# Kernel optimization log

Hardware: AMD Instinct MI355X
Metric: run time of the kernel (lower is better)

The kernel has to match this reference:

```python
import jax, jax.numpy as jnp
import numpy as np

N = 50000      # nodes
E = 800000     # edges (before self loops)
IN, H, OUT = 128, 64, 64
NEG_SLOPE = 0.2  # PyG GATConv leaky_relu slope


def _glorot(k, shape):
    lim = float(np.sqrt(6.0 / (shape[0] + shape[1])))
    return jax.random.uniform(k, shape, jnp.float32, -lim, lim)


def setup_inputs() -> dict:
    key = jax.random.key(0)
    ks = jax.random.split(key, 16)
    x = jax.random.normal(ks[0], (N, IN), jnp.float32)
    edge_src = jax.random.randint(ks[1], (E,), 0, N, jnp.int32)
    edge_dst = jax.random.randint(ks[2], (E,), 0, N, jnp.int32)
    dims = [(IN, H), (H, H), (H, OUT)]
    inp = {"x": x, "edge_src": edge_src, "edge_dst": edge_dst}
    i = 3
    for l, (di, do) in enumerate(dims):
        inp[f"W{l}"] = _glorot(ks[i], (di, do)); i += 1
        inp[f"as{l}"] = _glorot(ks[i], (1, do))[0]; i += 1
        inp[f"ad{l}"] = _glorot(ks[i], (1, do))[0]; i += 1
        inp[f"b{l}"] = jnp.zeros((do,), jnp.float32)
    return inp


def _gat_layer(x, W, a_src, a_dst, b, src, dst):
    # single-head GATConv (PyG semantics, self loops already in src/dst)
    h = x @ W                              # [N, do]
    s = h @ a_src                          # [N] source attention logits
    d = h @ a_dst                          # [N] dest attention logits
    e = jax.nn.leaky_relu(s[src] + d[dst], NEG_SLOPE)   # [E']
    # segment softmax over incoming edges of each destination node
    m = jax.ops.segment_max(e, dst, num_segments=N)
    w = jnp.exp(e - m[dst])
    denom = jax.ops.segment_sum(w, dst, num_segments=N)
    coef = w / (denom[dst] + 1e-16)
    out = jax.ops.segment_sum(h[src] * coef[:, None], dst, num_segments=N)
    return out + b


def reference(x, edge_src, edge_dst, W0, as0, ad0, b0, W1, as1, ad1, b1, W2, as2, ad2, b2):
    # add self loops (GATConv default add_self_loops=True)
    loop = jnp.arange(N, dtype=edge_src.dtype)
    src = jnp.concatenate([edge_src, loop])
    dst = jnp.concatenate([edge_dst, loop])
    h = jax.nn.relu(_gat_layer(x, W0, as0, ad0, b0, src, dst))
    # dropout is identity in eval mode
    h = jax.nn.relu(_gat_layer(h, W1, as1, ad1, b1, src, dst))
    return _gat_layer(h, W2, as2, ad2, b2, src, dst)
```

## Files before the change

### kernel.cpp

```cpp
#include <hip/hip_runtime.h>
#include <hip/hip_fp16.h>
#include <math.h>

#define WAVE 64
#define NEG_SLOPE 0.2f
#define LSTR 68


__global__ __launch_bounds__(256) void bucket_count_kernel(
    const int* __restrict__ dst, int* __restrict__ gcnt, int e, int nb) {
    extern __shared__ int cnt[];
    for (int b = threadIdx.x; b < nb; b += 256) cnt[b] = 0;
    __syncthreads();
    int base = blockIdx.x * 4096;
#pragma unroll
    for (int k = 0; k < 16; ++k) {
        int i = base + k * 256 + threadIdx.x;
        if (i < e) atomicAdd(&cnt[dst[i] >> 7], 1);
    }
    __syncthreads();
    for (int b = threadIdx.x; b < nb; b += 256) {
        int c = cnt[b];
        if (c) atomicAdd(&gcnt[b], c);
    }
}

__global__ __launch_bounds__(512) void bucket_scan_kernel(
    const int* __restrict__ gcnt, int* __restrict__ boff, int* __restrict__ gfill,
    int* __restrict__ rowptr, int nb, int e, int n) {
    __shared__ int sh[512];
    int t = threadIdx.x;
    int v = (t < nb) ? gcnt[t] : 0;
    sh[t] = v;
    __syncthreads();
    for (int o = 1; o < 512; o <<= 1) {
        int u = (t >= o) ? sh[t - o] : 0;
        __syncthreads();
        sh[t] += u;
        __syncthreads();
    }
    if (t < nb) { int ex = sh[t] - v; boff[t] = ex; gfill[t] = ex; }
    if (t == 0) { boff[nb] = e; rowptr[n] = e + n; }
}

__global__ __launch_bounds__(256) void bucket_place_kernel(
    const int* __restrict__ src, const int* __restrict__ dst,
    int* __restrict__ gfill, int* __restrict__ binned, int e, int nb) {
    extern __shared__ int lds[];
    int* cnt = lds;
    int* bas = lds + nb;
    for (int b = threadIdx.x; b < nb; b += 256) cnt[b] = 0;
    __syncthreads();
    int base = blockIdx.x * 4096;
#pragma unroll
    for (int k = 0; k < 16; ++k) {
        int i = base + k * 256 + threadIdx.x;
        if (i < e) atomicAdd(&cnt[dst[i] >> 7], 1);
    }
    __syncthreads();
    for (int b = threadIdx.x; b < nb; b += 256) {
        int c = cnt[b];
        bas[b] = c ? atomicAdd(&gfill[b], c) : 0;
        cnt[b] = 0;
    }
    __syncthreads();
#pragma unroll
    for (int k = 0; k < 16; ++k) {
        int i = base + k * 256 + threadIdx.x;
        if (i < e) {
            int d = dst[i];
            int bk = d >> 7;
            int r = atomicAdd(&cnt[bk], 1);
            binned[bas[bk] + r] = ((d & 127) << 16) | src[i];
        }
    }
}

__global__ __launch_bounds__(256) void bucket_build_kernel(
    const int* __restrict__ binned, const int* __restrict__ boff,
    int* __restrict__ csr_src, int* __restrict__ rowptr, int n) {
    __shared__ int cnt[128], off[128], pcnt[128];
    int b = blockIdx.x;
    int t = threadIdx.x;
    int nodeBase = b << 7;
    int nc = min(128, n - nodeBase);
    int e0 = boff[b], e1 = boff[b + 1];
    int ne = e1 - e0;
    if (t < 128) { cnt[t] = 1; pcnt[t] = 1; }
    __syncthreads();
    for (int i = t; i < ne; i += 256)
        atomicAdd(&cnt[binned[e0 + i] >> 16], 1);
    __syncthreads();
    if (t < 128) off[t] = cnt[t];
    __syncthreads();
    for (int o = 1; o < 128; o <<= 1) {
        int u = (t >= o && t < 128) ? off[t - o] : 0;
        __syncthreads();
        if (t < 128) off[t] += u;
        __syncthreads();
    }
    if (t < 128) off[t] -= cnt[t];
    __syncthreads();
    int csrBase = e0 + nodeBase;
    if (t < nc) {
        rowptr[nodeBase + t] = csrBase + off[t];
        csr_src[csrBase + off[t]] = nodeBase + t;
    }
    for (int i = t; i < ne; i += 256) {
        int p = binned[e0 + i];
        int loc = p >> 16;
        int r = atomicAdd(&pcnt[loc], 1);
        csr_src[csrBase + off[loc] + r] = p & 0xFFFF;
    }
}


template <int K>
__global__ __launch_bounds__(256) void gemm_feat_kernel(
    const float* __restrict__ X, const float* __restrict__ W,
    const float* __restrict__ a_s, const float* __restrict__ a_d,
    __half* __restrict__ H, float* __restrict__ S, float* __restrict__ D, int n) {
    __shared__ float Xs[64 * LSTR];
    __shared__ float Ws[64 * LSTR];
    int t = threadIdx.x;
    int tx = t & 15;
    int ty = t >> 4;
    int base = blockIdx.x * 64;
    float acc[4][4] = {};

    int q = t & 3;
    int srow = t >> 2;

    for (int k0 = 0; k0 < K; k0 += 64) {
        int grow = base + srow;
#pragma unroll
        for (int j = 0; j < 4; ++j) {
            int c = 16 * j + 4 * q;
            float4 v = make_float4(0.f, 0.f, 0.f, 0.f);
            if (grow < n) v = *(const float4*)(X + (size_t)grow * K + k0 + c);
            *(float4*)(Xs + srow * LSTR + c) = v;
            float4 w = *(const float4*)(W + (size_t)(k0 + srow) * 64 + c);
            *(float4*)(Ws + srow * LSTR + c) = w;
        }
        __syncthreads();
#pragma unroll 8
        for (int kk = 0; kk < 64; ++kk) {
            float4 wv = *(const float4*)(Ws + kk * LSTR + 4 * tx);
#pragma unroll
            for (int i = 0; i < 4; ++i) {
                float xv = Xs[(4 * ty + i) * LSTR + kk];
                acc[i][0] = fmaf(xv, wv.x, acc[i][0]);
                acc[i][1] = fmaf(xv, wv.y, acc[i][1]);
                acc[i][2] = fmaf(xv, wv.z, acc[i][2]);
                acc[i][3] = fmaf(xv, wv.w, acc[i][3]);
            }
        }
        __syncthreads();
    }

    const float4 av_s = *(const float4*)(a_s + 4 * tx);
    const float4 av_d = *(const float4*)(a_d + 4 * tx);
#pragma unroll
    for (int i = 0; i < 4; ++i) {
        int row = base + 4 * ty + i;
        bool ok = row < n;
        if (ok) {
            __half2 h01 = __floats2half2_rn(acc[i][0], acc[i][1]);
            __half2 h23 = __floats2half2_rn(acc[i][2], acc[i][3]);
            uint2 u;
            u.x = *(unsigned int*)&h01;
            u.y = *(unsigned int*)&h23;
            *(uint2*)(H + (size_t)row * 64 + 4 * tx) = u;
        }
        float ps = acc[i][0] * av_s.x + acc[i][1] * av_s.y +
                   acc[i][2] * av_s.z + acc[i][3] * av_s.w;
        float pd = acc[i][0] * av_d.x + acc[i][1] * av_d.y +
                   acc[i][2] * av_d.z + acc[i][3] * av_d.w;
        for (int o = 1; o < 16; o <<= 1) {
            ps += __shfl_xor(ps, o);
            pd += __shfl_xor(pd, o);
        }
        if (tx == 0 && ok) { S[row] = ps; D[row] = pd; }
    }
}


__global__ __launch_bounds__(256) void gat_aggregate_kernel(
    const __half* __restrict__ H, const float* __restrict__ S,
    const float* __restrict__ D, const int* __restrict__ rowptr,
    const int* __restrict__ csr_src, const float* __restrict__ bias,
    float* __restrict__ OUT, int n, int do_relu) {
    int wid  = (blockIdx.x * blockDim.x + threadIdx.x) >> 6;
    int lane = threadIdx.x & 63;
    if (wid >= n) return;
    int eg = lane >> 4;
    int cg = lane & 15;
    int start = rowptr[wid];
    int end   = rowptr[wid + 1];
    float d_i = D[wid];

    float z = 0.f;
    float4 acc = make_float4(0.f, 0.f, 0.f, 0.f);

    for (int cb = start; cb < end; cb += WAVE) {
        int j = cb + lane;
        bool v = j < end;
        int sc = v ? csr_src[j] : 0;
        float sv = S[sc];
        float e = sv + d_i;
        e = (e > 0.f) ? e : NEG_SLOPE * e;
        float w = v ? __expf(e) : 0.f;

        int nch = min(WAVE, end - cb);
        int rounds = (nch + 3) >> 2;
#pragma unroll 4
        for (int r = 0; r < rounds; ++r) {
            int idx = 4 * r + eg;
            float wr = __shfl(w, idx);
            int   sr = __shfl(sc, idx);
            float2 f0 = make_float2(0.f, 0.f), f1 = f0;
            if (idx < nch) {
                uint2 u = *(const uint2*)(H + (size_t)sr * 64 + 4 * cg);
                f0 = __half22float2(*(__half2*)&u.x);
                f1 = __half22float2(*(__half2*)&u.y);
            }
            z += wr;
            acc.x = fmaf(wr, f0.x, acc.x);
            acc.y = fmaf(wr, f0.y, acc.y);
            acc.z = fmaf(wr, f1.x, acc.z);
            acc.w = fmaf(wr, f1.y, acc.w);
        }
    }

    for (int o = 16; o < 64; o <<= 1) {
        acc.x += __shfl_xor(acc.x, o);
        acc.y += __shfl_xor(acc.y, o);
        acc.z += __shfl_xor(acc.z, o);
        acc.w += __shfl_xor(acc.w, o);
        z     += __shfl_xor(z, o);
    }

    if (eg == 0) {
        float inv = 1.f / (z + 1e-16f);
        const float4 bv = *(const float4*)(bias + 4 * cg);
        float4 o4;
        o4.x = acc.x * inv + bv.x;
        o4.y = acc.y * inv + bv.y;
        o4.z = acc.z * inv + bv.z;
        o4.w = acc.w * inv + bv.w;
        if (do_relu) {
            o4.x = fmaxf(o4.x, 0.f); o4.y = fmaxf(o4.y, 0.f);
            o4.z = fmaxf(o4.z, 0.f); o4.w = fmaxf(o4.w, 0.f);
        }
        *(float4*)(OUT + (size_t)wid * 64 + 4 * cg) = o4;
    }
}


static inline size_t align256(size_t x) { return (x + 255) & ~(size_t)255; }

extern "C" void kernel_launch(void* const* d_in, const int* in_sizes, int n_in,
                              void* d_out, int out_size, void* d_ws, size_t ws_size,
                              hipStream_t stream) {
    const float* x    = (const float*)d_in[0];
    const int*   esrc = (const int*)d_in[1];
    const int*   edst = (const int*)d_in[2];
    const int E = in_sizes[1];
    const int N = in_sizes[0] / 128;

    const float* W0 = (const float*)d_in[3];
    const float* as0 = (const float*)d_in[4];
    const float* ad0 = (const float*)d_in[5];
    const float* b0 = (const float*)d_in[6];
    const float* W1 = (const float*)d_in[7];
    const float* as1 = (const float*)d_in[8];
    const float* ad1 = (const float*)d_in[9];
    const float* b1 = (const float*)d_in[10];
    const float* W2 = (const float*)d_in[11];
    const float* as2 = (const float*)d_in[12];
    const float* ad2 = (const float*)d_in[13];
    const float* b2 = (const float*)d_in[14];

    const int NB = (N + 127) >> 7;

    char* p = (char*)d_ws;
    int* gcnt    = (int*)p; p += align256((size_t)(NB + 1) * 4);
    int* boff    = (int*)p; p += align256((size_t)(NB + 1) * 4);
    int* gfill   = (int*)p; p += align256((size_t)(NB + 1) * 4);
    int* rowptr  = (int*)p; p += align256((size_t)(N + 1) * 4);
    int* csr_src = (int*)p; p += align256((size_t)(E + N) * 4);
    int* binned  = (int*)p; p += align256((size_t)E * 4);
    __half* h16 = (__half*)p; p += align256((size_t)N * 64 * 2);
    float* sA = (float*)p; p += align256((size_t)N * 4);
    float* dA = (float*)p; p += align256((size_t)N * 4);
    float* XA = (float*)p; p += align256((size_t)N * 64 * 4);
    float* XB = (float*)p; p += align256((size_t)N * 64 * 4);
    float* out = (float*)d_out;

    int nchunk = (E + 4095) / 4096;
    hipMemsetAsync(gcnt, 0, (size_t)(NB + 1) * 4, stream);
    bucket_count_kernel<<<nchunk, 256, NB * 4, stream>>>(edst, gcnt, E, NB);
    bucket_scan_kernel<<<1, 512, 0, stream>>>(gcnt, boff, gfill, rowptr, NB, E, N);
    bucket_place_kernel<<<nchunk, 256, 2 * NB * 4, stream>>>(esrc, edst, gfill, binned, E, NB);
    bucket_build_kernel<<<NB, 256, 0, stream>>>(binned, boff, csr_src, rowptr, N);

    int tile_grid = (N + 63) / 64;
    int agg_grid  = (N + 3) / 4;

    gemm_feat_kernel<128><<<tile_grid, 256, 0, stream>>>(x, W0, as0, ad0, h16, sA, dA, N);
    gat_aggregate_kernel<<<agg_grid, 256, 0, stream>>>(h16, sA, dA, rowptr, csr_src, b0, XA, N, 1);

    gemm_feat_kernel<64><<<tile_grid, 256, 0, stream>>>(XA, W1, as1, ad1, h16, sA, dA, N);
    gat_aggregate_kernel<<<agg_grid, 256, 0, stream>>>(h16, sA, dA, rowptr, csr_src, b1, XB, N, 1);

    gemm_feat_kernel<64><<<tile_grid, 256, 0, stream>>>(XB, W2, as2, ad2, h16, sA, dA, N);
    gat_aggregate_kernel<<<agg_grid, 256, 0, stream>>>(h16, sA, dA, rowptr, csr_src, b2, out, N, 0);
}
```

Before: 271.2 us.

## Replace FP32 SIMT feature GEMM with FP16 MFMA matrix-core kernel

Rewrites the per-layer feature GEMM to convert X and W to fp16 in shared memory. It then computes 16x16 output tiles per wave with mfma_f32_16x16x32_f16 instead of the scalar FMA loop. W is stored transposed so both operands can be read as 8-wide fp16 vectors, and the full K is staged at once. The goal is to cut GEMM compute time. In exchange, the fp16 rounding of inputs adds error to the attention logits, and the H stores are now scalar halves instead of vector stores.

```diff
diff --git a/kernel.cpp b/kernel.cpp
--- a/kernel.cpp
+++ b/kernel.cpp
@@ -5,6 +5,9 @@
 #define WAVE 64
 #define NEG_SLOPE 0.2f
 #define LSTR 68
+
+typedef _Float16 half8 __attribute__((ext_vector_type(8)));
+typedef float f32x4 __attribute__((ext_vector_type(4)));
 
 
 __global__ __launch_bounds__(256) void bucket_count_kernel(
@@ -116,71 +119,85 @@
 
 
 template <int K>
-__global__ __launch_bounds__(256) void gemm_feat_kernel(
+__global__ __launch_bounds__(256) void mfma_gemm_feat_kernel(
     const float* __restrict__ X, const float* __restrict__ W,
     const float* __restrict__ a_s, const float* __restrict__ a_d,
     __half* __restrict__ H, float* __restrict__ S, float* __restrict__ D, int n) {
-    __shared__ float Xs[64 * LSTR];
-    __shared__ float Ws[64 * LSTR];
+    constexpr int AK = K + 8;
+    __shared__ _Float16 Xs[64 * AK];
+    __shared__ _Float16 Bt[64 * AK];
     int t = threadIdx.x;
-    int tx = t & 15;
-    int ty = t >> 4;
     int base = blockIdx.x * 64;
-    float acc[4][4] = {};
-
-    int q = t & 3;
-    int srow = t >> 2;
-
-    for (int k0 = 0; k0 < K; k0 += 64) {
-        int grow = base + srow;
-#pragma unroll
-        for (int j = 0; j < 4; ++j) {
-            int c = 16 * j + 4 * q;
-            float4 v = make_float4(0.f, 0.f, 0.f, 0.f);
-            if (grow < n) v = *(const float4*)(X + (size_t)grow * K + k0 + c);
-            *(float4*)(Xs + srow * LSTR + c) = v;
-            float4 w = *(const float4*)(W + (size_t)(k0 + srow) * 64 + c);
-            *(float4*)(Ws + srow * LSTR + c) = w;
-        }
-        __syncthreads();
-#pragma unroll 8
-        for (int kk = 0; kk < 64; ++kk) {
-            float4 wv = *(const float4*)(Ws + kk * LSTR + 4 * tx);
-#pragma unroll
-            for (int i = 0; i < 4; ++i) {
-                float xv = Xs[(4 * ty + i) * LSTR + kk];
-                acc[i][0] = fmaf(xv, wv.x, acc[i][0]);
-                acc[i][1] = fmaf(xv, wv.y, acc[i][1]);
-                acc[i][2] = fmaf(xv, wv.z, acc[i][2]);
-                acc[i][3] = fmaf(xv, wv.w, acc[i][3]);
+
+    {
+        int row = t >> 2, q = t & 3;
+        int grow = base + row;
+        constexpr int CW = K / 4;
+#pragma unroll
+        for (int c0 = 0; c0 < CW; c0 += 8) {
+            float4 v0 = make_float4(0.f, 0.f, 0.f, 0.f), v1 = v0;
+            if (grow < n) {
+                v0 = *(const float4*)(X + (size_t)grow * K + q * CW + c0);
+                v1 = *(const float4*)(X + (size_t)grow * K + q * CW + c0 + 4);
             }
-        }
-        __syncthreads();
-    }
-
-    const float4 av_s = *(const float4*)(a_s + 4 * tx);
-    const float4 av_d = *(const float4*)(a_d + 4 * tx);
-#pragma unroll
-    for (int i = 0; i < 4; ++i) {
-        int row = base + 4 * ty + i;
-        bool ok = row < n;
-        if (ok) {
-            __half2 h01 = __floats2half2_rn(acc[i][0], acc[i][1]);
-            __half2 h23 = __floats2half2_rn(acc[i][2], acc[i][3]);
-            uint2 u;
-            u.x = *(unsigned int*)&h01;
-            u.y = *(unsigned int*)&h23;
-            *(uint2*)(H + (size_t)row * 64 + 4 * tx) = u;
-        }
-        float ps = acc[i][0] * av_s.x + acc[i][1] * av_s.y +
-                   acc[i][2] * av_s.z + acc[i][3] * av_s.w;
-        float pd = acc[i][0] * av_d.x + acc[i][1] * av_d.y +
-                   acc[i][2] * av_d.z + acc[i][3] * av_d.w;
+            _Float16 h[8] = {(_Float16)v0.x, (_Float16)v0.y, (_Float16)v0.z, (_Float16)v0.w,
+                             (_Float16)v1.x, (_Float16)v1.y, (_Float16)v1.z, (_Float16)v1.w};
+            *(uint4*)(Xs + row * AK + q * CW + c0) = *(uint4*)h;
+        }
+    }
+    {
+        int nn = t & 63, g = t >> 6;
+        constexpr int KW = K / 4;
+        _Float16 hbuf[KW];
+#pragma unroll
+        for (int j = 0; j < KW; ++j)
+            hbuf[j] = (_Float16)W[(size_t)(g * KW + j) * 64 + nn];
+#pragma unroll
+        for (int j = 0; j < KW; j += 8)
+            *(uint4*)(Bt + nn * AK + g * KW + j) = *(uint4*)(hbuf + j);
+    }
+    __syncthreads();
+
+    int lane = t & 63;
+    int wv = t >> 6;
+    int m0 = wv * 16;
+    int l15 = lane & 15, quad = lane >> 4;
+
+    f32x4 acc[4] = {{0.f, 0.f, 0.f, 0.f}, {0.f, 0.f, 0.f, 0.f},
+                    {0.f, 0.f, 0.f, 0.f}, {0.f, 0.f, 0.f, 0.f}};
+#pragma unroll
+    for (int ks = 0; ks < K; ks += 32) {
+        half8 a = *(half8*)(Xs + (m0 + l15) * AK + ks + quad * 8);
+#pragma unroll
+        for (int cg = 0; cg < 4; ++cg) {
+            half8 b = *(half8*)(Bt + (cg * 16 + l15) * AK + ks + quad * 8);
+            acc[cg] = __builtin_amdgcn_mfma_f32_16x16x32_f16(a, b, acc[cg], 0, 0, 0);
+        }
+    }
+
+    float as_c[4], ad_c[4];
+#pragma unroll
+    for (int cg = 0; cg < 4; ++cg) {
+        as_c[cg] = a_s[cg * 16 + l15];
+        ad_c[cg] = a_d[cg * 16 + l15];
+    }
+#pragma unroll
+    for (int r = 0; r < 4; ++r) {
+        int grow = base + m0 + quad * 4 + r;
+        bool ok = grow < n;
+        float ps = 0.f, pd = 0.f;
+#pragma unroll
+        for (int cg = 0; cg < 4; ++cg) {
+            float v = acc[cg][r];
+            if (ok) H[(size_t)grow * 64 + cg * 16 + l15] = __float2half(v);
+            ps += v * as_c[cg];
+            pd += v * ad_c[cg];
+        }
         for (int o = 1; o < 16; o <<= 1) {
             ps += __shfl_xor(ps, o);
             pd += __shfl_xor(pd, o);
         }
-        if (tx == 0 && ok) { S[row] = ps; D[row] = pd; }
+        if (l15 == 0 && ok) { S[grow] = ps; D[grow] = pd; }
     }
 }
 
@@ -307,12 +324,12 @@
     int tile_grid = (N + 63) / 64;
     int agg_grid  = (N + 3) / 4;
 
-    gemm_feat_kernel<128><<<tile_grid, 256, 0, stream>>>(x, W0, as0, ad0, h16, sA, dA, N);
+    mfma_gemm_feat_kernel<128><<<tile_grid, 256, 0, stream>>>(x, W0, as0, ad0, h16, sA, dA, N);
     gat_aggregate_kernel<<<agg_grid, 256, 0, stream>>>(h16, sA, dA, rowptr, csr_src, b0, XA, N, 1);
 
-    gemm_feat_kernel<64><<<tile_grid, 256, 0, stream>>>(XA, W1, as1, ad1, h16, sA, dA, N);
+    mfma_gemm_feat_kernel<64><<<tile_grid, 256, 0, stream>>>(XA, W1, as1, ad1, h16, sA, dA, N);
     gat_aggregate_kernel<<<agg_grid, 256, 0, stream>>>(h16, sA, dA, rowptr, csr_src, b1, XB, N, 1);
 
-    gemm_feat_kernel<64><<<tile_grid, 256, 0, stream>>>(XB, W2, as2, ad2, h16, sA, dA, N);
+    mfma_gemm_feat_kernel<64><<<tile_grid, 256, 0, stream>>>(XB, W2, as2, ad2, h16, sA, dA, N);
     gat_aggregate_kernel<<<agg_grid, 256, 0, stream>>>(h16, sA, dA, rowptr, csr_src, b2, out, N, 0);
 }
```

Result: faster. 257.8 us (-4.9%).
